# Kernel tuning notes

Measured on AMD Instinct MI355X. Metric: run time of the kernel, lower is better.

The kernel has to match this reference:

```python
import jax, jax.numpy as jnp
import numpy as np

WS = [1024, 2048, 4096, 8192]
RS = [1, 2, 4, 8]
HEAD_IDX = 0
B, N, C, H = 4, 8192, 1024, 128


def setup_inputs() -> dict:
    key = jax.random.key(0)
    kx, kq, kk, kv = jax.random.split(key, 4)
    x = jax.random.normal(kx, (B, N, C), dtype=jnp.float32)
    # small init scale keeps exp(logits) well-conditioned, like trained weights
    Wq = jax.random.normal(kq, (C, H), dtype=jnp.float32) * 0.02
    Wk = jax.random.normal(kk, (C, H), dtype=jnp.float32) * 0.02
    Wv = jax.random.normal(kv, (C, H), dtype=jnp.float32) * 0.02
    return {"x": x, "Wq": Wq, "Wk": Wk, "Wv": Wv}


def _cfg_attention(x, Wq, Wk, Wv, w, r, offset):
    # one (window, dilation) config: strided gather -> causal attn per segment
    b, n, c = x.shape
    h = Wq.shape[1]
    S = n // w
    xs = x.reshape(b, S, w, c)[:, :, offset::r, :]  # [b,S,m,c] dilated sub-seqs
    m = xs.shape[2]
    q = jnp.einsum('bsmc,ch->bsmh', xs, Wq)
    k = jnp.einsum('bsmc,ch->bsmh', xs, Wk)
    v = jnp.einsum('bsmc,ch->bsmh', xs, Wv)
    scores = jnp.einsum('bsqh,bskh->bsqk', q, k) / jnp.sqrt(jnp.float32(h))
    causal = jnp.tril(jnp.ones((m, m), dtype=bool))
    scores = jnp.where(causal, scores, -jnp.inf)
    lse = jax.scipy.special.logsumexp(scores, axis=-1)       # [b,S,m]
    p = jnp.exp(scores - lse[..., None])                     # stable softmax
    o = jnp.einsum('bsqk,bskh->bsqh', p, v)                  # [b,S,m,h]
    denom = jnp.exp(lse)                                     # softmax denominator
    pos = (jnp.arange(S)[:, None] * w + offset
           + jnp.arange(m)[None, :] * r).reshape(-1)         # flat positions [S*m]
    return pos, o.reshape(b, S * m, h), denom.reshape(b, S * m)


def reference(x, Wq, Wk, Wv):
    b, n, _ = x.shape
    h = Wq.shape[1]
    denom_sums = jnp.zeros((b, n), dtype=x.dtype)
    cfgs = []
    for w, r in zip(WS, RS):
        offset = HEAD_IDX % r
        pos, o, denom = _cfg_attention(x, Wq, Wk, Wv, w, r, offset)
        denom_sums = denom_sums.at[:, pos].add(denom)  # cross-config denom sum
        cfgs.append((pos, o, denom))
    out = jnp.zeros((b, n, h), dtype=x.dtype)
    for pos, o, denom in cfgs:
        alpha = denom / denom_sums[:, pos]             # [b, S*m]
        out = out.at[:, pos, :].add(o * alpha[:, :, None])
    return out
```

## Files before the change

### kernel.cpp

```cpp
#include <hip/hip_runtime.h>

typedef __attribute__((ext_vector_type(8))) short s16x8;
typedef __attribute__((ext_vector_type(4))) short s16x4;
typedef __attribute__((ext_vector_type(4))) float f32x4;

#define MFMA16(a,b,c) __builtin_amdgcn_mfma_f32_16x16x32_bf16((a),(b),(c),0,0,0)

#define GLOAD_LDS16(g, l) \
    __builtin_amdgcn_global_load_lds((const __attribute__((address_space(1))) void*)(g), \
                                     (__attribute__((address_space(3))) void*)(l), 16, 0, 0)

__device__ __forceinline__ unsigned short f2bf(float f) {
    unsigned u = __builtin_bit_cast(unsigned, f);
    u = (u + 0x7FFFu + ((u >> 16) & 1u)) >> 16;
    return (unsigned short)u;
}

#define MB ((size_t)1 << 20)
#define WT_OFF   ((size_t)0)
#define QKV_OFF  (1*MB)
#define VT0_OFF  (25*MB)
#define VT1_OFF  (33*MB)
#define VT2_OFF  (37*MB)
#define VT3_OFF  (39*MB)
#define KG1_OFF  (40*MB)
#define KG2_OFF  (44*MB)
#define KG3_OFF  (46*MB)
#define O0_OFF   (47*MB)
#define O1_OFF   (63*MB)
#define O2_OFF   (71*MB)
#define O3_OFF   (75*MB)
#define L0_OFF   (77*MB)
#define L1_OFF   (L0_OFF + (size_t)131072)
#define L2_OFF   (L1_OFF + (size_t)65536)
#define L3_OFF   (L2_OFF + (size_t)32768)

__global__ __launch_bounds__(256) void k_wt(const float* __restrict__ Wq, const float* __restrict__ Wk,
                                            const float* __restrict__ Wv, unsigned short* __restrict__ Wt) {
    int id = blockIdx.x * 256 + threadIdx.x;
    int mat = id >> 17;
    int rem = id & 131071;
    int h = rem >> 10, c = rem & 1023;
    const float* W = (mat == 0) ? Wq : (mat == 1) ? Wk : Wv;
    Wt[id] = f2bf(W[c * 128 + h]);
}

__global__ __launch_bounds__(256, 2) void k_qkv(const float* __restrict__ x,
                                                const unsigned short* __restrict__ Wt,
                                                unsigned short* __restrict__ QKV) {
    union SMem {
        struct { float As[64][64]; unsigned short Bs[384][64]; } s;
        unsigned short Cs[64][392];
    };
    __shared__ SMem sm;
    float* Asf = &sm.s.As[0][0];
    unsigned short* Bsu = &sm.s.Bs[0][0];

    const int mt = blockIdx.x;
    const int tid = threadIdx.x, lane = tid & 63, wv = tid >> 6;
    const int quad = lane >> 4, m16 = lane & 15;
    const int wr = wv >> 1, wc = wv & 1;
    const float* xb = x + (size_t)mt * 64 * 1024;

    f32x4 acc[2][12];
#pragma unroll
    for (int i = 0; i < 2; i++)
#pragma unroll
        for (int j = 0; j < 12; j++) acc[i][j] = (f32x4)0.f;

    for (int kk = 0; kk < 1024; kk += 64) {
#pragma unroll
        for (int t = 0; t < 4; t++) {
            int id = wv * 4 + t;
            int row = id * 4 + (lane >> 4);
            int gl = (lane & 15) ^ (row & 7);
            GLOAD_LDS16(xb + (size_t)row * 1024 + kk + gl * 4, (char*)Asf + id * 1024);
        }
#pragma unroll
        for (int t = 0; t < 12; t++) {
            int id = wv * 12 + t;
            int col = id * 8 + (lane >> 3);
            int gl = (lane & 7) ^ (lane >> 3);
            GLOAD_LDS16(Wt + (size_t)col * 1024 + kk + gl * 8, (char*)Bsu + id * 1024);
        }
        __syncthreads();
#pragma unroll
        for (int c32 = 0; c32 < 2; c32++) {
            s16x8 a[2], b[12];
#pragma unroll
            for (int rt = 0; rt < 2; rt++) {
                int row = wr * 32 + rt * 16 + m16;
                int g0 = c32 * 8 + quad * 2;
                float4 lo = *(const float4*)&Asf[row * 64 + ((g0 ^ (row & 7)) << 2)];
                float4 hi = *(const float4*)&Asf[row * 64 + (((g0 + 1) ^ (row & 7)) << 2)];
                s16x8 av;
                av[0] = (short)f2bf(lo.x); av[1] = (short)f2bf(lo.y);
                av[2] = (short)f2bf(lo.z); av[3] = (short)f2bf(lo.w);
                av[4] = (short)f2bf(hi.x); av[5] = (short)f2bf(hi.y);
                av[6] = (short)f2bf(hi.z); av[7] = (short)f2bf(hi.w);
                a[rt] = av;
            }
#pragma unroll
            for (int ct = 0; ct < 12; ct++) {
                int col = wc * 192 + ct * 16 + m16;
                b[ct] = *(const s16x8*)&Bsu[col * 64 + (((c32 * 4 + quad) ^ (col & 7)) << 3)];
            }
#pragma unroll
            for (int rt = 0; rt < 2; rt++)
#pragma unroll
                for (int ct = 0; ct < 12; ct++) acc[rt][ct] = MFMA16(a[rt], b[ct], acc[rt][ct]);
        }
        __syncthreads();
    }

#pragma unroll
    for (int rt = 0; rt < 2; rt++)
#pragma unroll
        for (int ct = 0; ct < 12; ct++)
#pragma unroll
            for (int rg = 0; rg < 4; rg++)
                sm.Cs[wr * 32 + rt * 16 + quad * 4 + rg][wc * 192 + ct * 16 + m16] = f2bf(acc[rt][ct][rg]);
    __syncthreads();
#pragma unroll
    for (int i = 0; i < 12; i++) {
        int id = tid + 256 * i;
        int row = id / 48, cc = id % 48;
        int col = cc * 8, mat = col >> 7, h = col & 127;
        *(s16x8*)(QKV + (size_t)mat * 4194304 + ((size_t)(mt * 64 + row)) * 128 + h) =
            *(const s16x8*)&sm.Cs[row][col];
    }
}

__device__ __forceinline__ void decode_vt(int bid, int& c, int& b, int& s, int& t8) {
    int base;
    if (bid < 256)      { c = 0; base = 0; }
    else if (bid < 384) { c = 1; base = 256; }
    else if (bid < 448) { c = 2; base = 384; }
    else                { c = 3; base = 448; }
    int rem = bid - base;
    int sh = 6 - c;
    b = rem >> sh;
    int rr = rem & ((1 << sh) - 1);
    s = rr >> 3; t8 = rr & 7;
}

__global__ __launch_bounds__(256) void k_gather(const unsigned short* __restrict__ QKV, char* __restrict__ ws) {
    const unsigned short* K = QKV + (size_t)1 * 4194304;
    const unsigned short* V = QKV + (size_t)2 * 4194304;
    int bid = blockIdx.x, tid = threadIdx.x;
    if (bid < 480) {
        int c, b, s, kb; decode_vt(bid, c, b, s, kb);
        const int S = 8 >> c, r = 1 << c, wseg = 1024 << c;
        const size_t vtoff[4] = {VT0_OFF, VT1_OFF, VT2_OFF, VT3_OFF};
        unsigned short* Vt = (unsigned short*)(ws + vtoff[c]) + ((size_t)(b * S + s)) * 131072;
        int kq8 = tid & 15, hq = tid >> 4;
        int key0 = kb * 128 + kq8 * 8;
        int jt = key0 >> 6, k0 = key0 & 63;
        s16x8 in[8];
#pragma unroll
        for (int i = 0; i < 8; i++) {
            int tok = s * wseg + (key0 + i) * r;
            in[i] = *(const s16x8*)(V + ((size_t)(b * 8192 + tok)) * 128 + hq * 8);
        }
#pragma unroll
        for (int jh = 0; jh < 8; jh++) {
            s16x8 o;
#pragma unroll
            for (int i = 0; i < 8; i++) o[i] = in[i][jh];
            *(s16x8*)(Vt + (size_t)jt * 8192 + (size_t)(hq * 8 + jh) * 64 + k0) = o;
        }
    } else {
        int r2 = bid - 480, c;
        if (r2 < 128)      { c = 1; }
        else if (r2 < 192) { c = 2; r2 -= 128; }
        else               { c = 3; r2 -= 192; }
        const int S = 8 >> c, r = 1 << c, wseg = 1024 << c;
        int b = r2 >> (6 - c);
        int rem = r2 & ((1 << (6 - c)) - 1);
        int s = rem >> 3, kb = rem & 7;
        const size_t kgoff[4] = {0, KG1_OFF, KG2_OFF, KG3_OFF};
        unsigned short* Kg = (unsigned short*)(ws + kgoff[c]) + ((size_t)(b * S + s)) * 131072;
        int row = tid >> 1, hh = (tid & 1) * 64;
        const unsigned short* src = K + ((size_t)(b * 8192 + s * wseg + (kb * 128 + row) * r)) * 128 + hh;
        unsigned short* dst = Kg + ((size_t)(kb * 128 + row)) * 128 + hh;
#pragma unroll
        for (int i = 0; i < 8; i++)
            *(s16x8*)(dst + i * 8) = *(const s16x8*)(src + i * 8);
    }
}

__global__ __launch_bounds__(256, 3) void k_attn(const unsigned short* __restrict__ QKV,
                                                 char* __restrict__ ws) {
    __shared__ s16x8 KsV[1024];
    __shared__ s16x8 VsV[1024];
    __shared__ unsigned short Ps[128][72];

    const int segid = blockIdx.x & 63;
    if (segid >= 60) return;
    const int p = blockIdx.x >> 6;
    int c, b, s;
    if (segid < 32)      { c = 0; b = segid >> 3;        s = segid & 7; }
    else if (segid < 48) { c = 1; b = (segid - 32) >> 2; s = (segid - 32) & 3; }
    else if (segid < 56) { c = 2; b = (segid - 48) >> 1; s = (segid - 48) & 1; }
    else                 { c = 3; b = segid - 56;        s = 0; }
    const int S = 8 >> c, r = 1 << c, wseg = 1024 << c;
    const int segc = b * S + s;
    const int qtL = p, qtH = 15 - p, J = qtH + 1;

    const size_t vtoff[4] = {VT0_OFF, VT1_OFF, VT2_OFF, VT3_OFF};
    const size_t ooff[4]  = {O0_OFF, O1_OFF, O2_OFF, O3_OFF};
    const size_t loff[4]  = {L0_OFF, L1_OFF, L2_OFF, L3_OFF};
    const size_t kgoff[4] = {0, KG1_OFF, KG2_OFF, KG3_OFF};
    const unsigned short* Q  = QKV;
    const unsigned short* Kg = (c == 0)
        ? QKV + (size_t)1 * 4194304 + (size_t)segc * 131072
        : (const unsigned short*)(ws + kgoff[c]) + (size_t)segc * 131072;
    const unsigned short* Vt = (const unsigned short*)(ws + vtoff[c]) + (size_t)segc * 131072;
    float* Ob = (float*)(ws + ooff[c]) + (size_t)segc * 1024 * 128;
    float* Lb = (float*)(ws + loff[c]) + (size_t)segc * 1024;

    const int tid = threadIdx.x, lane = tid & 63, wv = tid >> 6;
    const int quad = lane >> 4, m16 = lane & 15;
    const float SCE = 0.08838834764831845f;

    s16x8 qfL[4], qfH[4];
    {
        int tokL = s * wseg + (qtL * 64 + wv * 16 + m16) * r;
        int tokH = s * wseg + (qtH * 64 + wv * 16 + m16) * r;
        const unsigned short* qpL = Q + ((size_t)(b * 8192 + tokL)) * 128;
        const unsigned short* qpH = Q + ((size_t)(b * 8192 + tokH)) * 128;
#pragma unroll
        for (int c4 = 0; c4 < 4; c4++) {
            qfL[c4] = *(const s16x8*)(qpL + c4 * 32 + quad * 8);
            qfH[c4] = *(const s16x8*)(qpH + c4 * 32 + quad * 8);
        }
    }
    f32x4 oaccL[8], oaccH[8];
#pragma unroll
    for (int i = 0; i < 8; i++) { oaccL[i] = (f32x4)0.f; oaccH[i] = (f32x4)0.f; }
    float lsumL[4] = {}, lsumH[4] = {};

    for (int j = 0; j < J; j++) {
        const unsigned short* Kgt = Kg + (size_t)j * 8192;
        const unsigned short* Vtt = Vt + (size_t)j * 8192;
#pragma unroll
        for (int t = 0; t < 8; t++) {
            int id = wv * 8 + t;
            if (id < 16) {
                int c4 = id >> 2, qd = id & 3;
                GLOAD_LDS16(Kgt + (size_t)lane * 128 + c4 * 32 + qd * 8, &KsV[id * 64]);
            } else {
                int v = id - 16;
                int kc = v >> 3, qd = (v >> 1) & 3, hh = v & 1;
                GLOAD_LDS16(Vtt + (size_t)(hh * 64 + lane) * 64 + kc * 32 + qd * 8,
                            &VsV[(kc * 4 + qd) * 128 + hh * 64]);
            }
        }
        __syncthreads();

        const bool lowA = (j <= qtL);
        const bool dgL = (j == qtL), dgH = (j == qtH);
        const int rbase = wv * 16 + quad * 4;
#pragma unroll
        for (int ct = 0; ct < 4; ct++) {
            f32x4 sL = (f32x4)0.f, sH = (f32x4)0.f;
#pragma unroll
            for (int c4 = 0; c4 < 4; c4++) {
                s16x8 kf = KsV[(c4 * 4 + quad) * 64 + ct * 16 + m16];
                if (lowA) sL = MFMA16(qfL[c4], kf, sL);
                sH = MFMA16(qfH[c4], kf, sH);
            }
            int colL = ct * 16 + m16;
            if (lowA) {
#pragma unroll
                for (int rg = 0; rg < 4; rg++) {
                    float pv = __expf(sL[rg] * SCE);
                    if (dgL && colL > rbase + rg) pv = 0.f;
                    lsumL[rg] += pv;
                    Ps[rbase + rg][colL] = f2bf(pv);
                }
            }
#pragma unroll
            for (int rg = 0; rg < 4; rg++) {
                float pv = __expf(sH[rg] * SCE);
                if (dgH && colL > rbase + rg) pv = 0.f;
                lsumH[rg] += pv;
                Ps[64 + rbase + rg][colL] = f2bf(pv);
            }
        }
#pragma unroll
        for (int kc = 0; kc < 2; kc++) {
            s16x8 aH = *(const s16x8*)&Ps[64 + wv * 16 + m16][kc * 32 + quad * 8];
            s16x8 aL;
            if (lowA) aL = *(const s16x8*)&Ps[wv * 16 + m16][kc * 32 + quad * 8];
#pragma unroll
            for (int nt = 0; nt < 8; nt++) {
                s16x8 bv = VsV[(kc * 4 + quad) * 128 + nt * 16 + m16];
                if (lowA) oaccL[nt] = MFMA16(aL, bv, oaccL[nt]);
                oaccH[nt] = MFMA16(aH, bv, oaccH[nt]);
            }
        }
        __syncthreads();
    }

#pragma unroll
    for (int rg = 0; rg < 4; rg++) {
        float vL = lsumL[rg], vH = lsumH[rg];
        vL += __shfl_xor(vL, 1); vL += __shfl_xor(vL, 2);
        vL += __shfl_xor(vL, 4); vL += __shfl_xor(vL, 8);
        vH += __shfl_xor(vH, 1); vH += __shfl_xor(vH, 2);
        vH += __shfl_xor(vH, 4); vH += __shfl_xor(vH, 8);
        lsumL[rg] = vL; lsumH[rg] = vH;
    }
    float* OcL = Ob + (size_t)(qtL * 64) * 128;
    float* OcH = Ob + (size_t)(qtH * 64) * 128;
#pragma unroll
    for (int nt = 0; nt < 8; nt++)
#pragma unroll
        for (int rg = 0; rg < 4; rg++) {
            int rl = wv * 16 + quad * 4 + rg;
            OcL[(size_t)rl * 128 + nt * 16 + m16] = oaccL[nt][rg];
            OcH[(size_t)rl * 128 + nt * 16 + m16] = oaccH[nt][rg];
        }
    if (m16 == 0) {
#pragma unroll
        for (int rg = 0; rg < 4; rg++) {
            int rl = wv * 16 + quad * 4 + rg;
            Lb[qtL * 64 + rl] = lsumL[rg];
            Lb[qtH * 64 + rl] = lsumH[rg];
        }
    }
}

__global__ __launch_bounds__(256) void k_combine(const char* __restrict__ ws, float* __restrict__ out) {
    int gid = blockIdx.x * 256 + threadIdx.x;
    int rown = gid >> 5;
    int h4 = (gid & 31) * 4;
    int b = rown >> 13, n = rown & 8191;
    const size_t ooff[4] = {O0_OFF, O1_OFF, O2_OFF, O3_OFF};
    const size_t loff[4] = {L0_OFF, L1_OFF, L2_OFF, L3_OFF};
    float denom = 0.f;
    float4 acc = {0.f, 0.f, 0.f, 0.f};
#pragma unroll
    for (int c = 0; c < 4; c++) {
        if ((n & ((1 << c) - 1)) == 0) {
            int s = n >> (10 + c);
            int i = (n & ((1024 << c) - 1)) >> c;
            int rowc = b * (8192 >> c) + (s << 10) + i;
            denom += *((const float*)(ws + loff[c]) + rowc);
            const float4 o = *(const float4*)((const float*)(ws + ooff[c]) + (size_t)rowc * 128 + h4);
            acc.x += o.x; acc.y += o.y; acc.z += o.z; acc.w += o.w;
        }
    }
    float inv = 1.f / denom;
    float4 res = {acc.x * inv, acc.y * inv, acc.z * inv, acc.w * inv};
    *(float4*)(out + (size_t)rown * 128 + h4) = res;
}

extern "C" void kernel_launch(void* const* d_in, const int* in_sizes, int n_in,
                              void* d_out, int out_size, void* d_ws, size_t ws_size,
                              hipStream_t stream) {
    const float* x  = (const float*)d_in[0];
    const float* Wq = (const float*)d_in[1];
    const float* Wk = (const float*)d_in[2];
    const float* Wv = (const float*)d_in[3];
    char* ws = (char*)d_ws;
    unsigned short* Wt  = (unsigned short*)(ws + WT_OFF);
    unsigned short* QKV = (unsigned short*)(ws + QKV_OFF);

    k_wt<<<1536, 256, 0, stream>>>(Wq, Wk, Wv, Wt);
    k_qkv<<<512, 256, 0, stream>>>(x, Wt, QKV);
    k_gather<<<704, 256, 0, stream>>>(QKV, ws);
    k_attn<<<512, 256, 0, stream>>>(QKV, ws);
    k_combine<<<4096, 256, 0, stream>>>(ws, (float*)d_out);
}
```

Before: 297.2 us.

## Pre-swizzle K and V tiles into fragment-contiguous layout for coalesced LDS loads

The gather kernel now writes both K (including config 0, which previously read K straight from the QKV buffer) and transposed V into a per-64-key-tile layout where each 16-byte fragment chunk is stored contiguously per lane. The attention kernel's global-to-LDS loads therefore become fully contiguous 512-element strides instead of scattered 128/64-element row strides. This aims to improve load coalescing in the hot attention loop. The cost is an extra gather pass for config 0's K, which needs 256 more gather blocks and a new workspace region.

```diff
diff --git a/kernel.cpp b/kernel.cpp
--- a/kernel.cpp
+++ b/kernel.cpp
@@ -34,6 +34,7 @@
 #define L1_OFF   (L0_OFF + (size_t)131072)
 #define L2_OFF   (L1_OFF + (size_t)65536)
 #define L3_OFF   (L2_OFF + (size_t)32768)
+#define KI0_OFF  (78*MB)
 
 __global__ __launch_bounds__(256) void k_wt(const float* __restrict__ Wq, const float* __restrict__ Wk,
                                             const float* __restrict__ Wv, unsigned short* __restrict__ Wt) {
@@ -167,25 +168,20 @@
             s16x8 o;
 #pragma unroll
             for (int i = 0; i < 8; i++) o[i] = in[i][jh];
-            *(s16x8*)(Vt + (size_t)jt * 8192 + (size_t)(hq * 8 + jh) * 64 + k0) = o;
+            *(s16x8*)(Vt + (size_t)jt * 8192 + (size_t)(k0 >> 3) * 1024 + (size_t)(hq * 8 + jh) * 8) = o;
         }
     } else {
-        int r2 = bid - 480, c;
-        if (r2 < 128)      { c = 1; }
-        else if (r2 < 192) { c = 2; r2 -= 128; }
-        else               { c = 3; r2 -= 192; }
+        int c, b, s, kb; decode_vt(bid - 480, c, b, s, kb);
         const int S = 8 >> c, r = 1 << c, wseg = 1024 << c;
-        int b = r2 >> (6 - c);
-        int rem = r2 & ((1 << (6 - c)) - 1);
-        int s = rem >> 3, kb = rem & 7;
-        const size_t kgoff[4] = {0, KG1_OFF, KG2_OFF, KG3_OFF};
-        unsigned short* Kg = (unsigned short*)(ws + kgoff[c]) + ((size_t)(b * S + s)) * 131072;
-        int row = tid >> 1, hh = (tid & 1) * 64;
-        const unsigned short* src = K + ((size_t)(b * 8192 + s * wseg + (kb * 128 + row) * r)) * 128 + hh;
-        unsigned short* dst = Kg + ((size_t)(kb * 128 + row)) * 128 + hh;
+        const size_t kioff[4] = {KI0_OFF, KG1_OFF, KG2_OFF, KG3_OFF};
+        unsigned short* Ki = (unsigned short*)(ws + kioff[c]) + ((size_t)(b * S + s)) * 131072;
+        int gkey = kb * 128 + (tid >> 1), hh = (tid & 1) * 64;
+        int jt = gkey >> 6, key = gkey & 63;
+        const unsigned short* src = K + ((size_t)(b * 8192 + s * wseg + gkey * r)) * 128 + hh;
+        unsigned short* dst = Ki + (size_t)jt * 8192 + (size_t)(hh >> 3) * 512 + key * 8;
 #pragma unroll
         for (int i = 0; i < 8; i++)
-            *(s16x8*)(dst + i * 8) = *(const s16x8*)(src + i * 8);
+            *(s16x8*)(dst + i * 512) = *(const s16x8*)(src + i * 8);
     }
 }
 
@@ -210,11 +206,9 @@
     const size_t vtoff[4] = {VT0_OFF, VT1_OFF, VT2_OFF, VT3_OFF};
     const size_t ooff[4]  = {O0_OFF, O1_OFF, O2_OFF, O3_OFF};
     const size_t loff[4]  = {L0_OFF, L1_OFF, L2_OFF, L3_OFF};
-    const size_t kgoff[4] = {0, KG1_OFF, KG2_OFF, KG3_OFF};
+    const size_t kioff[4] = {KI0_OFF, KG1_OFF, KG2_OFF, KG3_OFF};
     const unsigned short* Q  = QKV;
-    const unsigned short* Kg = (c == 0)
-        ? QKV + (size_t)1 * 4194304 + (size_t)segc * 131072
-        : (const unsigned short*)(ws + kgoff[c]) + (size_t)segc * 131072;
+    const unsigned short* Kg = (const unsigned short*)(ws + kioff[c]) + (size_t)segc * 131072;
     const unsigned short* Vt = (const unsigned short*)(ws + vtoff[c]) + (size_t)segc * 131072;
     float* Ob = (float*)(ws + ooff[c]) + (size_t)segc * 1024 * 128;
     float* Lb = (float*)(ws + loff[c]) + (size_t)segc * 1024;
@@ -247,13 +241,10 @@
         for (int t = 0; t < 8; t++) {
             int id = wv * 8 + t;
             if (id < 16) {
-                int c4 = id >> 2, qd = id & 3;
-                GLOAD_LDS16(Kgt + (size_t)lane * 128 + c4 * 32 + qd * 8, &KsV[id * 64]);
+                GLOAD_LDS16(Kgt + (size_t)id * 512 + lane * 8, &KsV[id * 64]);
             } else {
                 int v = id - 16;
-                int kc = v >> 3, qd = (v >> 1) & 3, hh = v & 1;
-                GLOAD_LDS16(Vtt + (size_t)(hh * 64 + lane) * 64 + kc * 32 + qd * 8,
-                            &VsV[(kc * 4 + qd) * 128 + hh * 64]);
+                GLOAD_LDS16(Vtt + (size_t)v * 512 + lane * 8, &VsV[v * 64]);
             }
         }
         __syncthreads();
@@ -370,7 +361,7 @@
 
     k_wt<<<1536, 256, 0, stream>>>(Wq, Wk, Wv, Wt);
     k_qkv<<<512, 256, 0, stream>>>(x, Wt, QKV);
-    k_gather<<<704, 256, 0, stream>>>(QKV, ws);
+    k_gather<<<960, 256, 0, stream>>>(QKV, ws);
     k_attn<<<512, 256, 0, stream>>>(QKV, ws);
     k_combine<<<4096, 256, 0, stream>>>(ws, (float*)d_out);
 }
```

Measured after the change: 280.3 us. -5.7%, faster.
